# Kernel tuning notes

Measured on AMD Instinct MI355X. Metric: run time of the kernel, lower is better.

## Reference

```python
import jax, jax.numpy as jnp
import numpy as np

B, NV, H, D = 8, 16, 192, 512
NH = 8
HD = D // NH
DFF = 2048
EPS = 1e-5


def _bn(x, g, b):
    # x: (N, T, C); BatchNorm1d over channel C using batch stats (train mode)
    mu = jnp.mean(x, axis=(0, 1))
    var = jnp.var(x, axis=(0, 1))
    return (x - mu) / jnp.sqrt(var + EPS) * g + b


def _ff(x, w1, b1, w2, b2):
    h = jax.nn.gelu(jnp.einsum('bnhd,fd->bnhf', x, w1) + b1, approximate=False)
    return jnp.einsum('bnhf,df->bnhd', h, w2) + b2


def setup_inputs() -> dict:
    key = jax.random.key(0)
    ks = jax.random.split(key, 20)
    s = 0.02
    return {
        'src': jax.random.normal(ks[0], (B, NV, H, D), jnp.float32),
        'qk_w': jax.random.normal(ks[1], (2 * D, D), jnp.float32) * s,
        'qk_b': jnp.zeros((2 * D,), jnp.float32),
        'v_w': jax.random.normal(ks[2], (D, D), jnp.float32) * s,
        'v_b': jnp.zeros((D,), jnp.float32),
        'alpha_p': jax.random.normal(ks[3], (HD, 1), jnp.float32) * 0.1,
        'g_pre1': jnp.ones((D,), jnp.float32),
        'b_pre1': jnp.zeros((D,), jnp.float32),
        'g_pre2': jnp.ones((D,), jnp.float32),
        'b_pre2': jnp.zeros((D,), jnp.float32),
        'ff1_w1': jax.random.normal(ks[4], (DFF, D), jnp.float32) * s,
        'ff1_b1': jnp.zeros((DFF,), jnp.float32),
        'ff1_w2': jax.random.normal(ks[5], (D, DFF), jnp.float32) * s,
        'ff1_b2': jnp.zeros((D,), jnp.float32),
        'ff2_w1': jax.random.normal(ks[6], (DFF, D), jnp.float32) * s,
        'ff2_b1': jnp.zeros((DFF,), jnp.float32),
        'ff2_w2': jax.random.normal(ks[7], (D, DFF), jnp.float32) * s,
        'ff2_b2': jnp.zeros((D,), jnp.float32),
        'g_attn': jnp.ones((D,), jnp.float32),
        'b_attn': jnp.zeros((D,), jnp.float32),
    }


def reference(src, qk_w, qk_b, v_w, v_b, alpha_p,
              g_pre1, b_pre1, g_pre2, b_pre2,
              ff1_w1, ff1_b1, ff1_w2, ff1_b2,
              ff2_w1, ff2_b1, ff2_w2, ff2_b2,
              g_attn, b_attn):
    b, n, h, c = src.shape
    hd = c // NH
    # normalized input for q,k; raw for v
    src1 = src / jnp.linalg.norm(src, axis=-1, keepdims=True)
    qk = (jnp.einsum('bnhc,ec->bnhe', src1, qk_w) + qk_b)
    qk = qk.reshape(b, n, h, 2, NH, hd).transpose(3, 0, 1, 4, 2, 5)  # (2,b,n,NH,h,hd)
    q, k = qk[0], qk[1]
    v = (jnp.einsum('bnhc,ec->bnhe', src, v_w) + v_b)
    v = v.reshape(b, n, h, NH, hd).transpose(0, 1, 3, 2, 4)  # (b,n,NH,h,hd)

    # exponential-decay weights in FFT domain (branch: h != 7)
    a = jax.nn.sigmoid(alpha_p)                  # (hd,1)
    ar = jnp.arange(h - 1, -1, -1, dtype=src.dtype)
    weights = a * (1.0 - a) ** ar                # (hd, h)
    n2 = 2 * h
    w_f = jnp.fft.rfft(weights, n=n2, axis=-1)   # (hd, h+1)
    q_f = jnp.swapaxes(jnp.fft.rfft(q, n=n2, axis=-2), -1, -2) * w_f
    k_f = jnp.swapaxes(jnp.fft.rfft(k, n=n2, axis=-2), -1, -2) * w_f
    q1 = jnp.swapaxes(jnp.fft.irfft(q_f, n=n2, axis=-1)[..., :h], -1, -2)
    k1 = jnp.swapaxes(jnp.fft.irfft(k_f, n=n2, axis=-1)[..., :h], -1, -2)

    # token-axis attention (note: original divides by head_dim**-0.5 == * sqrt(hd))
    score_t = jnp.einsum('bnhed,bnhfd->bnhef', q1, k1) * (hd ** 0.5)
    attn_t = jax.nn.softmax(score_t, axis=-1)
    out_tok = jnp.einsum('bnhef,bnhfd->bnhed', attn_t, v)  # (b,n,NH,h,hd)
    o3 = _bn(out_tok.reshape(b * n, h, NH * hd), g_pre2, b_pre2).reshape(b, n, h, c)

    # hidden-axis attention on un-decayed q,k (scale = sqrt(h))
    score_h = jnp.einsum('bnhae,bnhaf->bnhef', q, k) * (h ** 0.5)
    attn_h = jax.nn.softmax(score_h, axis=-1)
    out_hid = jnp.einsum('bnhef,bnhaf->bnhae', attn_h, v)  # (b,n,NH,h,hd)
    o2 = _bn(out_hid.reshape(b * n, h, NH * hd), g_pre1, b_pre1).reshape(b, n, h, c)

    src2 = _ff(o3, ff1_w1, ff1_b1, ff1_w2, ff1_b2) + _ff(o2, ff2_w1, ff2_b1, ff2_w2, ff2_b2)
    out = src + src2
    out = _bn(out.reshape(b * n, h, c), g_attn, b_attn).reshape(b, n, h, c)
    return out
```

## Files before the change

### kernel.cpp

```cpp
#include <hip/hip_runtime.h>
#include <math.h>

#define SEQ 192
#define NTOK 24576
#define EPS 1e-5f

typedef __bf16 bf16x8 __attribute__((ext_vector_type(8)));
typedef __bf16 bf16x4 __attribute__((ext_vector_type(4)));
typedef float  f32x4  __attribute__((ext_vector_type(4)));

__device__ __forceinline__ void load_lds16(const __bf16* g, __bf16* l) {
    __builtin_amdgcn_global_load_lds(
        (const __attribute__((address_space(1))) uint32_t*)g,
        (__attribute__((address_space(3))) uint32_t*)l, 16, 0, 0);
}

__device__ __forceinline__ float gelu_f(float x) {
    float z = 1.5957691216057308f * x * fmaf(0.044715f, x*x, 1.f);
    float e = __expf(-z);
    return x * __builtin_amdgcn_rcpf(1.f + e);
}

__global__ __launch_bounds__(256) void cvtprep_k(
    const float* __restrict__ s0, const float* __restrict__ s1, const float* __restrict__ s2,
    const float* __restrict__ s3, const float* __restrict__ s4, const float* __restrict__ s5,
    __bf16* __restrict__ dst,
    const float* __restrict__ src, __bf16* __restrict__ srcb, __bf16* __restrict__ srcnb)
{
    if (blockIdx.x < 4864) {
        int i = blockIdx.x * 256 + threadIdx.x;
        int f = i * 4;
        const float* s; int off;
        if      (f <  524288) { s = s0; off = 0;       }
        else if (f <  786432) { s = s1; off = 524288;  }
        else if (f < 1835008) { s = s2; off = 786432;  }
        else if (f < 2883584) { s = s3; off = 1835008; }
        else if (f < 3932160) { s = s4; off = 2883584; }
        else                  { s = s5; off = 3932160; }
        f32x4 v = *(const f32x4*)&s[f - off];
        bf16x4 o;
        o[0]=(__bf16)v[0]; o[1]=(__bf16)v[1]; o[2]=(__bf16)v[2]; o[3]=(__bf16)v[3];
        ((bf16x4*)dst)[i] = o;
    } else {
        int blk = blockIdx.x - 4864;
        int w = threadIdx.x >> 6, lane = threadIdx.x & 63;
        size_t token = blk * 4 + w;
        const float* p = src + token * 512 + lane * 8;
        f32x4 a0 = *(const f32x4*)p;
        f32x4 a1 = *(const f32x4*)(p + 4);
        float s = a0[0]*a0[0]+a0[1]*a0[1]+a0[2]*a0[2]+a0[3]*a0[3]
                + a1[0]*a1[0]+a1[1]*a1[1]+a1[2]*a1[2]+a1[3]*a1[3];
#pragma unroll
        for (int off = 32; off; off >>= 1) s += __shfl_xor(s, off);
        float rs = rsqrtf(s);
        bf16x8 vb, vn;
#pragma unroll
        for (int q = 0; q < 4; q++) {
            vb[q]   = (__bf16)a0[q];      vn[q]   = (__bf16)(a0[q]*rs);
            vb[q+4] = (__bf16)a1[q];      vn[q+4] = (__bf16)(a1[q]*rs);
        }
        *(bf16x8*)&srcb[token*512 + lane*8]  = vb;
        *(bf16x8*)&srcnb[token*512 + lane*8] = vn;
    }
}

template<bool GELU, bool DUAL>
__global__ __launch_bounds__(256) void gemm_k(
    const __bf16* __restrict__ A, const __bf16* __restrict__ B, __bf16* __restrict__ C,
    int N, int K, const float* __restrict__ bias,
    const __bf16* __restrict__ A2, const __bf16* __restrict__ B2, __bf16* __restrict__ C2,
    const float* __restrict__ bias2, int M1)
{
    __shared__ __bf16 As[8192];
    __shared__ __bf16 Bs[8192];
    const int tid = threadIdx.x, lane = tid & 63, w = tid >> 6;
    const int wr = w >> 1, wc = w & 1;
    const int b = blockIdx.y * gridDim.x + blockIdx.x;
    const int xcd = b & 7, bi = b >> 3;
    const int ypx = gridDim.y >> 3;
    int m0 = (xcd * ypx + bi / gridDim.x) * 128;
    const int n0 = (bi % gridDim.x) * 128;
    if (DUAL && m0 >= M1) { A = A2; B = B2; C = C2; bias = bias2; m0 -= M1; }
    const int fr = lane & 15, fq = lane >> 4;
    const int grow = 8*w + (lane >> 3);
    const int gcol = ((lane & 7) ^ (lane >> 3)) * 8;
    const __bf16* gB = B + (size_t)(n0 + grow) * K + gcol;
    const __bf16* gA = A + (size_t)(m0 + grow) * K + gcol;
    __bf16* ldsA = As + 8*w*64 + lane*8;
    __bf16* ldsB = Bs + 8*w*64 + lane*8;

    f32x4 acc[4][4];
#pragma unroll
    for (int i = 0; i < 4; i++)
#pragma unroll
        for (int j = 0; j < 4; j++) acc[i][j] = (f32x4){0.f,0.f,0.f,0.f};

    for (int k0 = 0; k0 < K; k0 += 64) {
#pragma unroll
        for (int i = 0; i < 4; i++)
            load_lds16(gA + k0 + (size_t)(32*i)*K, ldsA + i*2048);
#pragma unroll
        for (int i = 0; i < 4; i++)
            load_lds16(gB + k0 + (size_t)(32*i)*K, ldsB + i*2048);
        __syncthreads();
#pragma unroll
        for (int kk = 0; kk < 2; kk++) {
            bf16x8 af[4], bfv[4];
#pragma unroll
            for (int i = 0; i < 4; i++)
                af[i] = *(bf16x8*)&As[(wr*64 + i*16 + fr)*64 + (((kk*4+fq) ^ (fr&7))*8)];
#pragma unroll
            for (int j = 0; j < 4; j++)
                bfv[j] = *(bf16x8*)&Bs[(wc*64 + j*16 + fr)*64 + (((kk*4+fq) ^ (fr&7))*8)];
#pragma unroll
            for (int i = 0; i < 4; i++)
#pragma unroll
                for (int j = 0; j < 4; j++)
                    acc[i][j] = __builtin_amdgcn_mfma_f32_16x16x32_bf16(af[i], bfv[j], acc[i][j], 0, 0, 0);
        }
        __syncthreads();
    }
    const int r4 = lane >> 4, cc = lane & 15;
#pragma unroll
    for (int i = 0; i < 4; i++) {
#pragma unroll
        for (int r = 0; r < 4; r++) {
            int m = m0 + wr*64 + i*16 + r4*4 + r;
#pragma unroll
            for (int j = 0; j < 4; j++) {
                int n = n0 + wc*64 + j*16 + cc;
                float v = acc[i][j][r] + bias[n];
                if (GELU) v = gelu_f(v);
                C[(size_t)m * N + n] = (__bf16)v;
            }
        }
    }
}

__global__ __launch_bounds__(256) void w1scale_k(
    __bf16* __restrict__ w1a, __bf16* __restrict__ w1b, const float* __restrict__ coef01,
    const float* __restrict__ b1in, const float* __restrict__ b2in,
    float* __restrict__ b1out, float* __restrict__ b2out)
{
    const int half = blockIdx.x >> 9;
    __bf16* wbase = half ? w1b : w1a;
    const float* coef = coef01 + half*1024;
    const float* bin  = half ? b2in  : b1in;
    float* bout       = half ? b2out : b1out;
    const int wv = threadIdx.x >> 6, lane = threadIdx.x & 63;
    const int n = (blockIdx.x & 511) * 4 + wv;
    __bf16* p = wbase + (size_t)n * 512 + lane * 8;
    bf16x8 v = *(bf16x8*)p;
    f32x4 sc0 = *(const f32x4*)(coef + lane*8);
    f32x4 sc1 = *(const f32x4*)(coef + lane*8 + 4);
    f32x4 sh0 = *(const f32x4*)(coef + 512 + lane*8);
    f32x4 sh1 = *(const f32x4*)(coef + 512 + lane*8 + 4);
    float dot = 0.f;
    bf16x8 o;
#pragma unroll
    for (int q = 0; q < 4; q++) {
        float w0 = (float)v[q], w1 = (float)v[q+4];
        o[q]   = (__bf16)(w0 * sc0[q]);
        o[q+4] = (__bf16)(w1 * sc1[q]);
        dot = fmaf(w0, sh0[q], dot);
        dot = fmaf(w1, sh1[q], dot);
    }
    *(bf16x8*)p = o;
#pragma unroll
    for (int off = 32; off; off >>= 1) dot += __shfl_xor(dot, off);
    if (lane == 0) bout[n] = bin[n] + dot;
}

__global__ __launch_bounds__(256) void gemm2_k(
    const __bf16* __restrict__ A1, const __bf16* __restrict__ A2,
    const __bf16* __restrict__ B1, const __bf16* __restrict__ B2,
    float* __restrict__ C, const float* __restrict__ b1, const float* __restrict__ b2,
    const float* __restrict__ resid, float* __restrict__ st)
{
    __shared__ __bf16 As[2][4096];
    __shared__ __bf16 Bs[2][8192];
    const int tid = threadIdx.x, lane = tid & 63, w = tid >> 6;
    const int wr = w >> 1, wc = w & 1;
    const int vb = blockIdx.x;
    const int xcd = vb & 7, k2 = vb >> 3;
    const int m0 = (xcd*24 + (k2 >> 2)) * 64;
    const int n0 = (k2 & 3) * 128;
    const int fr = lane & 15, fq = lane >> 4;
    const int grow = 8*w + (lane >> 3);
    const int gcol = ((lane & 7) ^ (lane >> 3)) * 8;
    const int K = 2048;
    const int ldsoff = 8*w*64 + lane*8;
    const __bf16* gA1 = A1 + (size_t)(m0 + grow) * K + gcol;
    const __bf16* gA2 = A2 + (size_t)(m0 + grow) * K + gcol;
    const __bf16* gB1 = B1 + (size_t)(n0 + grow) * K + gcol;
    const __bf16* gB2 = B2 + (size_t)(n0 + grow) * K + gcol;

#define G2_STAGE(pb, it_) do {                                              \
        int half_ = (it_) >> 5, k0_ = ((it_) & 31) * 64;                    \
        const __bf16* ga_ = (half_ ? gA2 : gA1) + k0_;                      \
        const __bf16* gb_ = (half_ ? gB2 : gB1) + k0_;                      \
        load_lds16(ga_,                  &As[pb][ldsoff]);                  \
        load_lds16(ga_ + (size_t)32*K,   &As[pb][ldsoff + 2048]);           \
        load_lds16(gb_,                  &Bs[pb][ldsoff]);                  \
        load_lds16(gb_ + (size_t)32*K,   &Bs[pb][ldsoff + 2048]);           \
        load_lds16(gb_ + (size_t)64*K,   &Bs[pb][ldsoff + 4096]);           \
        load_lds16(gb_ + (size_t)96*K,   &Bs[pb][ldsoff + 6144]);           \
    } while (0)

    f32x4 acc[2][4];
#pragma unroll
    for (int i = 0; i < 2; i++)
#pragma unroll
        for (int j = 0; j < 4; j++) acc[i][j] = (f32x4){0.f,0.f,0.f,0.f};

    G2_STAGE(0, 0);
    asm volatile("s_waitcnt vmcnt(0)" ::: "memory");
    __syncthreads();
    for (int it = 0; it < 64; ++it) {
        const int cur = it & 1;
        if (it + 1 < 64) G2_STAGE(cur ^ 1, it + 1);
#pragma unroll
        for (int kk = 0; kk < 2; kk++) {
            bf16x8 af[2], bfv[4];
#pragma unroll
            for (int i = 0; i < 2; i++)
                af[i] = *(bf16x8*)&As[cur][(wr*32 + i*16 + fr)*64 + (((kk*4+fq) ^ (fr&7))*8)];
#pragma unroll
            for (int j = 0; j < 4; j++)
                bfv[j] = *(bf16x8*)&Bs[cur][(wc*64 + j*16 + fr)*64 + (((kk*4+fq) ^ (fr&7))*8)];
#pragma unroll
            for (int i = 0; i < 2; i++)
#pragma unroll
                for (int j = 0; j < 4; j++)
                    acc[i][j] = __builtin_amdgcn_mfma_f32_16x16x32_bf16(af[i], bfv[j], acc[i][j], 0, 0, 0);
        }
        asm volatile("s_waitcnt vmcnt(0)" ::: "memory");
        __syncthreads();
    }
#undef G2_STAGE

    const int r4 = lane >> 4, cc = lane & 15;
    float cs[4] = {0,0,0,0}, cq[4] = {0,0,0,0};
#pragma unroll
    for (int i = 0; i < 2; i++) {
#pragma unroll
        for (int r = 0; r < 4; r++) {
            int m = m0 + wr*32 + i*16 + r4*4 + r;
#pragma unroll
            for (int j = 0; j < 4; j++) {
                int n = n0 + wc*64 + j*16 + cc;
                size_t idx = (size_t)m * 512 + n;
                float v = acc[i][j][r] + b1[n] + b2[n] + resid[idx];
                C[idx] = v;
                cs[j] += v; cq[j] = fmaf(v, v, cq[j]);
            }
        }
    }
#pragma unroll
    for (int j = 0; j < 4; j++) {
        cs[j] += __shfl_xor(cs[j], 16); cs[j] += __shfl_xor(cs[j], 32);
        cq[j] += __shfl_xor(cq[j], 16); cq[j] += __shfl_xor(cq[j], 32);
    }
    if (r4 == 0) {
#pragma unroll
        for (int j = 0; j < 4; j++) {
            int n = n0 + wc*64 + j*16 + cc;
            atomicAdd(&st[n], cs[j]);
            atomicAdd(&st[512 + n], cq[j]);
        }
    }
}

__device__ __forceinline__ void hidden_attn_body(
    const __bf16* __restrict__ QKb, const __bf16* __restrict__ Vb, __bf16* __restrict__ OHb,
    __bf16* smem, int bn, int nh)
{
    __bf16* Qt = smem;
    __bf16* Kt = smem + 12800;
    __bf16* Ps = smem;
    __bf16* Vs = smem + 4608;
    const int tid = threadIdx.x, lane = tid & 63, w = tid >> 6;
    const int fr = lane & 15, fq = lane >> 4;
    const size_t rowbase = (size_t)bn * SEQ;

#pragma unroll
    for (int it = 0; it < 12; it++) {
        int tk = tid + (it % 6) * 256;
        int j = tk & 63, tg = tk >> 6;
        const __bf16* gsrc = QKb + (rowbase + tg*8)*1024 + nh*64 + j + (it >= 6 ? 512 : 0);
        bf16x8 v;
#pragma unroll
        for (int u = 0; u < 8; u++) v[u] = gsrc[(size_t)u*1024];
        __bf16* dst = (it >= 6 ? Kt : Qt) + j*200 + tg*8;
        *(bf16x8*)dst = v;
    }
    __syncthreads();

    f32x4 acc[4];
#pragma unroll
    for (int i = 0; i < 4; i++) acc[i] = (f32x4){0.f,0.f,0.f,0.f};
#pragma unroll
    for (int kc = 0; kc < 6; kc++) {
        bf16x8 a = *(bf16x8*)&Qt[(w*16 + fr)*200 + kc*32 + fq*8];
#pragma unroll
        for (int nt = 0; nt < 4; nt++) {
            bf16x8 b = *(bf16x8*)&Kt[(nt*16 + fr)*200 + kc*32 + fq*8];
            acc[nt] = __builtin_amdgcn_mfma_f32_16x16x32_bf16(a, b, acc[nt], 0, 0, 0);
        }
    }
    const float sc = 13.856406460551018f;
    float pn[4][4];
#pragma unroll
    for (int reg = 0; reg < 4; reg++) {
        float m = -1e30f;
#pragma unroll
        for (int nt = 0; nt < 4; nt++) { acc[nt][reg] *= sc; m = fmaxf(m, acc[nt][reg]); }
#pragma unroll
        for (int off = 1; off < 16; off <<= 1) m = fmaxf(m, __shfl_xor(m, off));
        float l = 0.f;
#pragma unroll
        for (int nt = 0; nt < 4; nt++) { pn[nt][reg] = __expf(acc[nt][reg] - m); l += pn[nt][reg]; }
#pragma unroll
        for (int off = 1; off < 16; off <<= 1) l += __shfl_xor(l, off);
        float inv = 1.f / l;
#pragma unroll
        for (int nt = 0; nt < 4; nt++) pn[nt][reg] *= inv;
    }
    __syncthreads();
#pragma unroll
    for (int nt = 0; nt < 4; nt++)
#pragma unroll
        for (int reg = 0; reg < 4; reg++)
            Ps[(w*16 + fq*4 + reg)*72 + nt*16 + fr] = (__bf16)pn[nt][reg];
    for (int i = tid; i < 1536; i += 256) {
        int t = i >> 3, s = i & 7;
        *(bf16x8*)&Vs[t*72 + s*8] = *(const bf16x8*)&Vb[(rowbase+t)*512 + nh*64 + s*8];
    }
    __syncthreads();

    f32x4 o[3][4];
#pragma unroll
    for (int i = 0; i < 3; i++)
#pragma unroll
        for (int j = 0; j < 4; j++) o[i][j] = (f32x4){0.f,0.f,0.f,0.f};
#pragma unroll
    for (int kc = 0; kc < 2; kc++) {
        bf16x8 av[3];
#pragma unroll
        for (int mt = 0; mt < 3; mt++)
            av[mt] = *(bf16x8*)&Vs[(48*w + mt*16 + fr)*72 + kc*32 + fq*8];
#pragma unroll
        for (int nt = 0; nt < 4; nt++) {
            bf16x8 b = *(bf16x8*)&Ps[(nt*16 + fr)*72 + kc*32 + fq*8];
#pragma unroll
            for (int mt = 0; mt < 3; mt++)
                o[mt][nt] = __builtin_amdgcn_mfma_f32_16x16x32_bf16(av[mt], b, o[mt][nt], 0, 0, 0);
        }
    }
    __bf16* obase = OHb + ((size_t)(bn*8 + nh)) * SEQ * 64;
#pragma unroll
    for (int mt = 0; mt < 3; mt++)
#pragma unroll
        for (int reg = 0; reg < 4; reg++) {
            int t = 48*w + mt*16 + fq*4 + reg;
#pragma unroll
            for (int nt = 0; nt < 4; nt++)
                obase[(size_t)t*64 + nt*16 + fr] = (__bf16)o[mt][nt][reg];
        }
}

__device__ __forceinline__ void token_attn_body(
    const __bf16* __restrict__ QKb, const __bf16* __restrict__ Vb, __bf16* __restrict__ OT,
    const float* __restrict__ alpha, __bf16* smem, int bn, int nh)
{
    __bf16* Qs = smem;
    __bf16* Ks = smem + 13824;
    __bf16* Vt = smem;
    __bf16* Pw = smem + 12800;
    const int tid = threadIdx.x, lane = tid & 63, w = tid >> 6;
    const int fr = lane & 15, fq = lane >> 4;
    const size_t rowbase = (size_t)bn * SEQ;

    for (int i = tid; i < 1536; i += 256) {
        int t = i >> 3, s = i & 7;
        const __bf16* g = QKb + (rowbase + t)*1024 + nh*64;
        *(bf16x8*)&Qs[t*72 + s*8] = *(const bf16x8*)&g[s*8];
        *(bf16x8*)&Ks[t*72 + s*8] = *(const bf16x8*)&g[512 + s*8];
    }
    __syncthreads();

    if (tid < 128) {
        const int d = tid & 63;
        __bf16* col = (tid < 64) ? (Qs + d) : (Ks + d);
        const float av = 1.f / (1.f + __expf(-alpha[d]));
        const float r = 1.f - av;
        float P = 0.f, pw = 1.f;
#pragma unroll 4
        for (int t = 0; t < SEQ; t++) {
            P = fmaf(pw, (float)col[t*72], P);
            col[t*72] = (__bf16)P;
            pw *= r;
        }
        float f = av;
#pragma unroll 4
        for (int t = SEQ-1; t >= 0; t--) {
            col[t*72] = (__bf16)((float)col[t*72] * f);
            f *= r;
        }
    }
    __syncthreads();

    f32x4 S[3][12];
#pragma unroll
    for (int i = 0; i < 3; i++)
#pragma unroll
        for (int j = 0; j < 12; j++) S[i][j] = (f32x4){0.f,0.f,0.f,0.f};
#pragma unroll
    for (int kc = 0; kc < 2; kc++) {
        bf16x8 aq[3];
#pragma unroll
        for (int mt = 0; mt < 3; mt++)
            aq[mt] = *(bf16x8*)&Qs[(48*w + mt*16 + fr)*72 + kc*32 + fq*8];
#pragma unroll
        for (int nt = 0; nt < 12; nt++) {
            bf16x8 b = *(bf16x8*)&Ks[(nt*16 + fr)*72 + kc*32 + fq*8];
#pragma unroll
            for (int mt = 0; mt < 3; mt++)
                S[mt][nt] = __builtin_amdgcn_mfma_f32_16x16x32_bf16(aq[mt], b, S[mt][nt], 0, 0, 0);
        }
    }
#pragma unroll
    for (int mt = 0; mt < 3; mt++)
#pragma unroll
        for (int reg = 0; reg < 4; reg++) {
            float m = -1e30f;
#pragma unroll
            for (int nt = 0; nt < 12; nt++) { S[mt][nt][reg] *= 8.f; m = fmaxf(m, S[mt][nt][reg]); }
#pragma unroll
            for (int off = 1; off < 16; off <<= 1) m = fmaxf(m, __shfl_xor(m, off));
            float l = 0.f;
#pragma unroll
            for (int nt = 0; nt < 12; nt++) { S[mt][nt][reg] = __expf(S[mt][nt][reg] - m); l += S[mt][nt][reg]; }
#pragma unroll
            for (int off = 1; off < 16; off <<= 1) l += __shfl_xor(l, off);
            float inv = 1.f / l;
#pragma unroll
            for (int nt = 0; nt < 12; nt++) S[mt][nt][reg] *= inv;
        }
    __syncthreads();
#pragma unroll
    for (int it = 0; it < 6; it++) {
        int tk = tid + it * 256;
        int d = tk & 63, tg = tk >> 6;
        const __bf16* gsrc = Vb + (rowbase + tg*8)*512 + nh*64 + d;
        bf16x8 v;
#pragma unroll
        for (int u = 0; u < 8; u++) v[u] = gsrc[(size_t)u*512];
        *(bf16x8*)&Vt[d*200 + tg*8] = v;
    }
    __syncthreads();

    f32x4 O[3][4];
#pragma unroll
    for (int i = 0; i < 3; i++)
#pragma unroll
        for (int j = 0; j < 4; j++) O[i][j] = (f32x4){0.f,0.f,0.f,0.f};
    __bf16* myP = Pw + w*3456;
#pragma unroll
    for (int fc = 0; fc < 3; fc++) {
#pragma unroll
        for (int mt = 0; mt < 3; mt++)
#pragma unroll
            for (int j = 0; j < 4; j++)
#pragma unroll
                for (int reg = 0; reg < 4; reg++)
                    myP[(mt*16 + fq*4 + reg)*72 + j*16 + fr] = (__bf16)S[mt][fc*4 + j][reg];
#pragma unroll
        for (int kc = 0; kc < 2; kc++) {
            bf16x8 ap[3];
#pragma unroll
            for (int mt = 0; mt < 3; mt++)
                ap[mt] = *(bf16x8*)&myP[(mt*16 + fr)*72 + kc*32 + fq*8];
#pragma unroll
            for (int dt = 0; dt < 4; dt++) {
                bf16x8 b = *(bf16x8*)&Vt[(dt*16 + fr)*200 + fc*64 + kc*32 + fq*8];
#pragma unroll
                for (int mt = 0; mt < 3; mt++)
                    O[mt][dt] = __builtin_amdgcn_mfma_f32_16x16x32_bf16(ap[mt], b, O[mt][dt], 0, 0, 0);
            }
        }
    }
    __bf16* obase = OT + ((size_t)(bn*8 + nh)) * SEQ * 64;
#pragma unroll
    for (int mt = 0; mt < 3; mt++)
#pragma unroll
        for (int reg = 0; reg < 4; reg++) {
            int e = 48*w + mt*16 + fq*4 + reg;
#pragma unroll
            for (int dt = 0; dt < 4; dt++)
                obase[(size_t)e*64 + dt*16 + fr] = (__bf16)O[mt][dt][reg];
        }
}

__global__ __launch_bounds__(256) void attn_both_k(
    const __bf16* __restrict__ QKb, const __bf16* __restrict__ Vb,
    __bf16* __restrict__ OHb, __bf16* __restrict__ OT, const float* __restrict__ alpha)
{
    __shared__ __bf16 smem[27648];
    const int b = blockIdx.x;
    const int type = (b >> 8) & 1;
    const int idx = (b >> 9) * 256 + (b & 255);
    const int bn = idx >> 3, nh = idx & 7;
    if (type == 0) hidden_attn_body(QKb, Vb, OHb, smem, bn, nh);
    else           token_attn_body(QKb, Vb, OT, alpha, smem, bn, nh);
}

__global__ __launch_bounds__(256) void bn_stats1_k(const __bf16* __restrict__ x0,
    const __bf16* __restrict__ x1, float* __restrict__ part)
{
    __shared__ float red[3072];
    const __bf16* x = (blockIdx.x < 256) ? x0 : x1;
    const int blk = blockIdx.x & 255;
    const int col8 = threadIdx.x & 63;
    const int rl   = threadIdx.x >> 6;
    const size_t r0 = (size_t)blk * 96;
    f32x4 sA = {0,0,0,0}, sB = {0,0,0,0}, qA = {0,0,0,0}, qB = {0,0,0,0};
    for (int r = rl; r < 96; r += 4) {
        bf16x8 v = *(const bf16x8*)&x[(r0 + r)*512 + col8*8];
        f32x4 lo = { (float)v[0], (float)v[1], (float)v[2], (float)v[3] };
        f32x4 hi = { (float)v[4], (float)v[5], (float)v[6], (float)v[7] };
        sA += lo; sB += hi;
        qA += lo*lo; qB += hi*hi;
    }
    if (rl > 0) {
        float* p = &red[(rl-1)*1024];
        *(f32x4*)&p[col8*8]       = sA;  *(f32x4*)&p[col8*8 + 4]       = sB;
        *(f32x4*)&p[512 + col8*8] = qA;  *(f32x4*)&p[512 + col8*8 + 4] = qB;
    }
    __syncthreads();
    if (rl == 0) {
#pragma unroll
        for (int k = 0; k < 3; k++) {
            float* p = &red[k*1024];
            sA += *(f32x4*)&p[col8*8];       sB += *(f32x4*)&p[col8*8 + 4];
            qA += *(f32x4*)&p[512 + col8*8]; qB += *(f32x4*)&p[512 + col8*8 + 4];
        }
        float* o = &part[(size_t)blockIdx.x * 1024];
        *(f32x4*)&o[col8*8]       = sA;  *(f32x4*)&o[col8*8 + 4]       = sB;
        *(f32x4*)&o[512 + col8*8] = qA;  *(f32x4*)&o[512 + col8*8 + 4] = qB;
    }
}

__global__ __launch_bounds__(256) void bn_stats2_k(const float* __restrict__ part, float* __restrict__ st)
{
    int c = blockIdx.x * 256 + threadIdx.x;
    int half = c >> 10, cc = c & 1023;
    const float* p = part + (size_t)half * 262144;
    float s0 = 0.f, s1 = 0.f, s2 = 0.f, s3 = 0.f;
    for (int b = 0; b < 256; b += 4) {
        s0 += p[(size_t)b*1024 + cc];
        s1 += p[(size_t)(b+1)*1024 + cc];
        s2 += p[(size_t)(b+2)*1024 + cc];
        s3 += p[(size_t)(b+3)*1024 + cc];
    }
    st[c] = (s0 + s1) + (s2 + s3);
}

__global__ void bn_coef_k(const float* __restrict__ st,
                          const float* __restrict__ gA, const float* __restrict__ bA,
                          const float* __restrict__ gB, const float* __restrict__ bB,
                          float* __restrict__ coef)
{
    int tidx = threadIdx.x;
    int half = tidx >> 9, c = tidx & 511;
    const float* sb = st + half*1024;
    const float* g = half ? gB : gA;
    const float* b = half ? bB : bA;
    float* co = coef + half*1024;
    float mean = sb[c] * (1.f/24576.f);
    float var  = sb[512+c] * (1.f/24576.f) - mean*mean;
    float sc = rsqrtf(var + EPS) * g[c];
    co[c] = sc;
    co[512 + c] = b[c] - mean * sc;
}

__global__ __launch_bounds__(256) void bn_apply4_k(const float* __restrict__ x, const float* __restrict__ st,
    const float* __restrict__ g, const float* __restrict__ b, float* __restrict__ out)
{
    size_t i = (size_t)blockIdx.x * 256 + threadIdx.x;
    int col4 = i & 127;
    f32x4 v = ((const f32x4*)x)[i];
    f32x4 sm = ((const f32x4*)st)[col4];
    f32x4 sq = ((const f32x4*)(st + 512))[col4];
    f32x4 o;
#pragma unroll
    for (int j = 0; j < 4; j++) {
        int c = col4*4 + j;
        float mean = sm[j] * (1.f/24576.f);
        float var  = sq[j] * (1.f/24576.f) - mean*mean;
        o[j] = (v[j] - mean) * rsqrtf(var + EPS) * g[c] + b[c];
    }
    ((f32x4*)out)[i] = o;
}

extern "C" void kernel_launch(void* const* d_in, const int* in_sizes, int n_in,
                              void* d_out, int out_size, void* d_ws, size_t ws_size,
                              hipStream_t stream)
{
    const float* src    = (const float*)d_in[0];
    const float* qk_w   = (const float*)d_in[1];
    const float* qk_b   = (const float*)d_in[2];
    const float* v_w    = (const float*)d_in[3];
    const float* v_b    = (const float*)d_in[4];
    const float* alpha  = (const float*)d_in[5];
    const float* g_pre1 = (const float*)d_in[6];
    const float* b_pre1 = (const float*)d_in[7];
    const float* g_pre2 = (const float*)d_in[8];
    const float* b_pre2 = (const float*)d_in[9];
    const float* ff1_w1 = (const float*)d_in[10];
    const float* ff1_b1 = (const float*)d_in[11];
    const float* ff1_w2 = (const float*)d_in[12];
    const float* ff1_b2 = (const float*)d_in[13];
    const float* ff2_w1 = (const float*)d_in[14];
    const float* ff2_b1 = (const float*)d_in[15];
    const float* ff2_w2 = (const float*)d_in[16];
    const float* ff2_b2 = (const float*)d_in[17];
    const float* g_attn = (const float*)d_in[18];
    const float* b_attn = (const float*)d_in[19];
    float* out = (float*)d_out;

    __bf16* wq   = (__bf16*)d_ws;
    __bf16* wv   = wq  + 524288;
    __bf16* w11  = wv  + 262144;
    __bf16* w12  = w11 + 1048576;
    __bf16* w21  = w12 + 1048576;
    __bf16* w22  = w21 + 1048576;
    __bf16* srcb  = w22 + 1048576;
    __bf16* srcnb = srcb + (size_t)NTOK*512;
    __bf16* QKb   = srcnb + (size_t)NTOK*512;
    __bf16* Vb    = QKb + (size_t)NTOK*1024;
    __bf16* OHbf  = Vb + (size_t)NTOK*512;
    __bf16* o3bf  = OHbf + (size_t)NTOK*512;
    float*  stats = (float*)(o3bf + (size_t)NTOK*512);
    float*  coef0 = stats + 3072;
    float*  part0 = coef0 + 2048;
    float*  bias1p = part0 + 2*262144;
    float*  bias2p = bias1p + 2048;
    __bf16* H1 = srcb;
    __bf16* H2 = H1 + (size_t)12288*2048;
    float *st2 = stats + 2048;

    hipMemsetAsync(st2, 0, 1024*sizeof(float), stream);

    cvtprep_k<<<4864 + NTOK/4, 256, 0, stream>>>(qk_w, v_w, ff1_w1, ff1_w2, ff2_w1, ff2_w2, wq,
                                                 src, srcb, srcnb);

    gemm_k<false,false><<<dim3(8, 192), 256, 0, stream>>>(srcnb, wq, QKb, 1024, 512, qk_b,
                                                          nullptr, nullptr, nullptr, nullptr, 0);
    gemm_k<false,false><<<dim3(4, 192), 256, 0, stream>>>(srcb,  wv, Vb,  512,  512, v_b,
                                                          nullptr, nullptr, nullptr, nullptr, 0);

    attn_both_k<<<2048, 256, 0, stream>>>(QKb, Vb, OHbf, o3bf, alpha);

    bn_stats1_k<<<512, 256, 0, stream>>>(o3bf, OHbf, part0);
    bn_stats2_k<<<8, 256, 0, stream>>>(part0, stats);
    bn_coef_k<<<1, 1024, 0, stream>>>(stats, g_pre2, b_pre2, g_pre1, b_pre1, coef0);
    w1scale_k<<<1024, 256, 0, stream>>>(w11, w21, coef0, ff1_b1, ff2_b1, bias1p, bias2p);

    for (int ch = 0; ch < 2; ch++) {
        size_t off = (size_t)ch * 12288 * 512;
        gemm_k<true,true><<<dim3(16, 192), 256, 0, stream>>>(o3bf + off, w11, H1, 2048, 512, bias1p,
                                                             OHbf + off, w21, H2, bias2p, 12288);
        gemm2_k<<<768, 256, 0, stream>>>(H1, H2, w12, w22, out + off,
                                         ff1_b2, ff2_b2, src + off, st2);
    }

    bn_apply4_k<<<12288, 256, 0, stream>>>(out, st2, g_attn, b_attn, out);
}
```

Measured before the change: 668.1 us.

## Swizzle Q/K shared layout and pack softmax probs to bf16 to raise occupancy

Replaces the padded 72-stride Q/K shared-memory layout with an unpadded 64-stride XOR-swizzled layout, which shrinks the shared buffer while still avoiding bank conflicts. The score computation now runs one m-tile at a time and packs the softmax probabilities into bf16 registers, halving the live register footprint of the score matrix. A launch-bounds minimum of 3 blocks per CU is added so the compiler targets higher occupancy. The risk is register spills under the tighter bound, plus a shared-memory overlap between Pw and the smaller Ks region that needs checking.

```diff
diff --git a/kernel.cpp b/kernel.cpp
--- a/kernel.cpp
+++ b/kernel.cpp
@@ -374,7 +374,7 @@
     const float* __restrict__ alpha, __bf16* smem, int bn, int nh)
 {
     __bf16* Qs = smem;
-    __bf16* Ks = smem + 13824;
+    __bf16* Ks = smem + 12288;
     __bf16* Vt = smem;
     __bf16* Pw = smem + 12800;
     const int tid = threadIdx.x, lane = tid & 63, w = tid >> 6;
@@ -384,69 +384,75 @@
     for (int i = tid; i < 1536; i += 256) {
         int t = i >> 3, s = i & 7;
         const __bf16* g = QKb + (rowbase + t)*1024 + nh*64;
-        *(bf16x8*)&Qs[t*72 + s*8] = *(const bf16x8*)&g[s*8];
-        *(bf16x8*)&Ks[t*72 + s*8] = *(const bf16x8*)&g[512 + s*8];
+        int sw = t*64 + ((s ^ (t & 7)) * 8);
+        *(bf16x8*)&Qs[sw] = *(const bf16x8*)&g[s*8];
+        *(bf16x8*)&Ks[sw] = *(const bf16x8*)&g[512 + s*8];
     }
     __syncthreads();
 
     if (tid < 128) {
         const int d = tid & 63;
-        __bf16* col = (tid < 64) ? (Qs + d) : (Ks + d);
+        __bf16* base = (tid < 64) ? Qs : Ks;
+        const int dhi = d >> 3, dlo = d & 7;
         const float av = 1.f / (1.f + __expf(-alpha[d]));
         const float r = 1.f - av;
         float P = 0.f, pw = 1.f;
 #pragma unroll 4
         for (int t = 0; t < SEQ; t++) {
-            P = fmaf(pw, (float)col[t*72], P);
-            col[t*72] = (__bf16)P;
+            int a = t*64 + ((dhi ^ (t & 7)) << 3) + dlo;
+            P = fmaf(pw, (float)base[a], P);
+            base[a] = (__bf16)P;
             pw *= r;
         }
         float f = av;
 #pragma unroll 4
         for (int t = SEQ-1; t >= 0; t--) {
-            col[t*72] = (__bf16)((float)col[t*72] * f);
+            int a = t*64 + ((dhi ^ (t & 7)) << 3) + dlo;
+            base[a] = (__bf16)((float)base[a] * f);
             f *= r;
         }
     }
     __syncthreads();
 
-    f32x4 S[3][12];
-#pragma unroll
-    for (int i = 0; i < 3; i++)
-#pragma unroll
-        for (int j = 0; j < 12; j++) S[i][j] = (f32x4){0.f,0.f,0.f,0.f};
-#pragma unroll
-    for (int kc = 0; kc < 2; kc++) {
-        bf16x8 aq[3];
-#pragma unroll
-        for (int mt = 0; mt < 3; mt++)
-            aq[mt] = *(bf16x8*)&Qs[(48*w + mt*16 + fr)*72 + kc*32 + fq*8];
-#pragma unroll
-        for (int nt = 0; nt < 12; nt++) {
-            bf16x8 b = *(bf16x8*)&Ks[(nt*16 + fr)*72 + kc*32 + fq*8];
-#pragma unroll
-            for (int mt = 0; mt < 3; mt++)
-                S[mt][nt] = __builtin_amdgcn_mfma_f32_16x16x32_bf16(aq[mt], b, S[mt][nt], 0, 0, 0);
-        }
-    }
-#pragma unroll
-    for (int mt = 0; mt < 3; mt++)
+    bf16x4 p16[3][12];
+#pragma unroll
+    for (int mt = 0; mt < 3; mt++) {
+        f32x4 S[12];
+#pragma unroll
+        for (int j = 0; j < 12; j++) S[j] = (f32x4){0.f,0.f,0.f,0.f};
+#pragma unroll
+        for (int kc = 0; kc < 2; kc++) {
+            bf16x8 aq = *(bf16x8*)&Qs[(48*w + mt*16 + fr)*64 + (((kc*4+fq) ^ (fr&7))*8)];
+#pragma unroll
+            for (int nt = 0; nt < 12; nt++) {
+                bf16x8 b = *(bf16x8*)&Ks[(nt*16 + fr)*64 + (((kc*4+fq) ^ (fr&7))*8)];
+                S[nt] = __builtin_amdgcn_mfma_f32_16x16x32_bf16(aq, b, S[nt], 0, 0, 0);
+            }
+        }
 #pragma unroll
         for (int reg = 0; reg < 4; reg++) {
             float m = -1e30f;
 #pragma unroll
-            for (int nt = 0; nt < 12; nt++) { S[mt][nt][reg] *= 8.f; m = fmaxf(m, S[mt][nt][reg]); }
+            for (int nt = 0; nt < 12; nt++) { S[nt][reg] *= 8.f; m = fmaxf(m, S[nt][reg]); }
 #pragma unroll
             for (int off = 1; off < 16; off <<= 1) m = fmaxf(m, __shfl_xor(m, off));
             float l = 0.f;
 #pragma unroll
-            for (int nt = 0; nt < 12; nt++) { S[mt][nt][reg] = __expf(S[mt][nt][reg] - m); l += S[mt][nt][reg]; }
+            for (int nt = 0; nt < 12; nt++) { S[nt][reg] = __expf(S[nt][reg] - m); l += S[nt][reg]; }
 #pragma unroll
             for (int off = 1; off < 16; off <<= 1) l += __shfl_xor(l, off);
             float inv = 1.f / l;
 #pragma unroll
-            for (int nt = 0; nt < 12; nt++) S[mt][nt][reg] *= inv;
-        }
+            for (int nt = 0; nt < 12; nt++) S[nt][reg] *= inv;
+        }
+#pragma unroll
+        for (int nt = 0; nt < 12; nt++) {
+            bf16x4 v;
+#pragma unroll
+            for (int reg = 0; reg < 4; reg++) v[reg] = (__bf16)S[nt][reg];
+            p16[mt][nt] = v;
+        }
+    }
     __syncthreads();
 #pragma unroll
     for (int it = 0; it < 6; it++) {
@@ -474,7 +480,7 @@
             for (int j = 0; j < 4; j++)
 #pragma unroll
                 for (int reg = 0; reg < 4; reg++)
-                    myP[(mt*16 + fq*4 + reg)*72 + j*16 + fr] = (__bf16)S[mt][fc*4 + j][reg];
+                    myP[(mt*16 + fq*4 + reg)*72 + j*16 + fr] = p16[mt][fc*4 + j][reg];
 #pragma unroll
         for (int kc = 0; kc < 2; kc++) {
             bf16x8 ap[3];
@@ -502,11 +508,11 @@
         }
 }
 
-__global__ __launch_bounds__(256) void attn_both_k(
+__global__ __launch_bounds__(256, 3) void attn_both_k(
     const __bf16* __restrict__ QKb, const __bf16* __restrict__ Vb,
     __bf16* __restrict__ OHb, __bf16* __restrict__ OT, const float* __restrict__ alpha)
 {
-    __shared__ __bf16 smem[27648];
+    __shared__ __bf16 smem[26624];
     const int b = blockIdx.x;
     const int type = (b >> 8) & 1;
     const int idx = (b >> 9) * 256 + (b & 255);
```

Result: slower. 702.3 us (+5.1%).
